# Optimization experiments

Measured on AMD Instinct MI355X. Metric: run time of the kernel, lower is better.

## Reference

```python
import jax, jax.numpy as jnp
import numpy as np

B, N, C, D = 16, 1024, 768, 384

def setup_inputs() -> dict:
    key = jax.random.key(0)
    ks = jax.random.split(key, 12)
    s_in = 1.0 / np.sqrt(C)
    s_d = 1.0 / np.sqrt(D)
    return {
        "x": jax.random.normal(ks[0], (B, N, C), dtype=jnp.float32),
        "adj": jax.random.uniform(ks[1], (B, N, N), dtype=jnp.float32),
        "W_theta": jax.random.uniform(ks[2], (C, D), minval=-s_in, maxval=s_in),
        "b_theta": jax.random.uniform(ks[3], (D,), minval=-s_in, maxval=s_in),
        "W_phi": jax.random.uniform(ks[4], (C, D), minval=-s_in, maxval=s_in),
        "b_phi": jax.random.uniform(ks[5], (D,), minval=-s_in, maxval=s_in),
        "W_g": jax.random.uniform(ks[6], (C, D), minval=-s_in, maxval=s_in),
        "b_g": jax.random.uniform(ks[7], (D,), minval=-s_in, maxval=s_in),
        "W_out": jax.random.uniform(ks[8], (D, C), minval=-s_d, maxval=s_d),
        "b_out": jax.random.uniform(ks[9], (C,), minval=-s_d, maxval=s_d),
    }

def reference(x, adj, W_theta, b_theta, W_phi, b_phi, W_g, b_g, W_out, b_out):
    # projections: [B,N,C] @ [C,D] -> [B,N,D]
    theta = x @ W_theta + b_theta
    phi = x @ W_phi + b_phi
    g = x @ W_g + b_g
    # unscaled attention scores with multiplicative adjacency mask
    attn = jnp.einsum('bnd,bmd->bnm', theta, phi) * adj  # [B,N,N]
    attn = jax.nn.softmax(attn, axis=-1)  # dropout is identity in eval mode
    out = jnp.einsum('bnm,bmd->bnd', attn, g)  # [B,N,D]
    out = out @ W_out + b_out  # [B,N,C]
    return out + x
```

## Files before the change

kernel.cpp:

```cpp
#include <hip/hip_runtime.h>
#include <hip/hip_bf16.h>

typedef __hip_bfloat16 bf16;
typedef short bf16x8 __attribute__((ext_vector_type(8)));
typedef float f32x4 __attribute__((ext_vector_type(4)));

constexpr int Bb = 16, Nn = 1024, Cc = 768, Dd = 384;

static __device__ __forceinline__ f32x4 mfma16(bf16x8 a, bf16x8 b, f32x4 c) {
    return __builtin_amdgcn_mfma_f32_16x16x32_bf16(a, b, c, 0, 0, 0);
}
static __device__ __forceinline__ short f2b(float v) {
    __hip_bfloat16 h = __float2bfloat16(v);
    return *reinterpret_cast<short*>(&h);
}
static __device__ __forceinline__ float b2f(bf16 x) { return __bfloat162float(x); }
static __device__ __forceinline__ float ldf(const float* p) { return *p; }
static __device__ __forceinline__ float ldf(const bf16* p) { return __bfloat162float(*p); }

__global__ __launch_bounds__(256) void transpose_cast(
    const float* __restrict__ in, bf16* __restrict__ out, int K, int N)
{
    __shared__ float t[32][33];
    const int n0 = blockIdx.x * 32, k0 = blockIdx.y * 32;
    const int tx = threadIdx.x & 31, ty = threadIdx.x >> 5;
#pragma unroll
    for (int i = 0; i < 4; i++)
        t[ty + i * 8][tx] = in[(size_t)(k0 + ty + i * 8) * N + n0 + tx];
    __syncthreads();
#pragma unroll
    for (int i = 0; i < 4; i++)
        out[(size_t)(n0 + ty + i * 8) * K + k0 + tx] = __float2bfloat16(t[tx][ty + i * 8]);
}

template <typename TA, int EPI>
__global__ __launch_bounds__(256) void gemm_mfma(
    const TA* __restrict__ A, const bf16* __restrict__ BT,
    const float* __restrict__ bias, const float* __restrict__ resid,
    void* __restrict__ outp, int K, int Nout)
{
    __shared__ short As[128 * 40];
    __shared__ short Bs[128 * 40];
    const int tid = threadIdx.x;
    const int lane = tid & 63, w = tid >> 6;
    const int quad = lane >> 4, c = lane & 15;
    const int row0 = blockIdx.x * 128, col0 = blockIdx.y * 128;
    const int wm = (w & 1) * 64, wn = (w >> 1) * 64;

    const f32x4 fz = {0.f, 0.f, 0.f, 0.f};
    f32x4 acc[4][4];
#pragma unroll
    for (int i = 0; i < 4; i++)
#pragma unroll
        for (int j = 0; j < 4; j++) acc[i][j] = fz;

    for (int k0 = 0; k0 < K; k0 += 32) {
        __syncthreads();
        if (sizeof(TA) == 4) {
            const float* Af = (const float*)A;
#pragma unroll
            for (int u = 0; u < 4; u++) {
                const int id = u * 256 + tid;
                const int r = id >> 3, c4 = (id & 7) * 4;
                const float4 v = *reinterpret_cast<const float4*>(Af + (size_t)(row0 + r) * K + k0 + c4);
                uint2 p;
                p.x = ((unsigned)(unsigned short)f2b(v.y) << 16) | (unsigned short)(unsigned)f2b(v.x);
                p.y = ((unsigned)(unsigned short)f2b(v.w) << 16) | (unsigned short)(unsigned)f2b(v.z);
                *reinterpret_cast<uint2*>(&As[r * 40 + c4]) = p;
            }
        } else {
            const bf16* Ab = (const bf16*)A;
#pragma unroll
            for (int u = 0; u < 2; u++) {
                const int id = u * 256 + tid;
                const int r = id >> 2, c8 = (id & 3) * 8;
                const uint4 v = *reinterpret_cast<const uint4*>(Ab + (size_t)(row0 + r) * K + k0 + c8);
                *reinterpret_cast<uint4*>(&As[r * 40 + c8]) = v;
            }
        }
#pragma unroll
        for (int u = 0; u < 2; u++) {
            const int id = u * 256 + tid;
            const int r = id >> 2, c8 = (id & 3) * 8;
            const uint4 v = *reinterpret_cast<const uint4*>(BT + (size_t)(col0 + r) * K + k0 + c8);
            *reinterpret_cast<uint4*>(&Bs[r * 40 + c8]) = v;
        }
        __syncthreads();

        bf16x8 af[4], bfr[4];
#pragma unroll
        for (int i = 0; i < 4; i++)
            af[i] = *reinterpret_cast<const bf16x8*>(&As[(wm + i * 16 + c) * 40 + quad * 8]);
#pragma unroll
        for (int j = 0; j < 4; j++)
            bfr[j] = *reinterpret_cast<const bf16x8*>(&Bs[(wn + j * 16 + c) * 40 + quad * 8]);
#pragma unroll
        for (int i = 0; i < 4; i++)
#pragma unroll
            for (int j = 0; j < 4; j++)
                acc[i][j] = mfma16(af[i], bfr[j], acc[i][j]);
    }

#pragma unroll
    for (int i = 0; i < 4; i++) {
        const int rowb = row0 + wm + i * 16 + quad * 4;
#pragma unroll
        for (int j = 0; j < 4; j++) {
            const int col = col0 + wn + j * 16 + c;
            const float bcol = bias[col];
#pragma unroll
            for (int r = 0; r < 4; r++) {
                float v = acc[i][j][r] + bcol;
                const int rr = rowb + r;
                if (EPI == 0) {
                    ((bf16*)outp)[(size_t)rr * Nout + col] = __float2bfloat16(v);
                } else if (EPI == 1) {
                    const int bb = rr >> 10, m = rr & 1023;
                    ((bf16*)outp)[((size_t)(bb * Nout + col)) * 1024 + m] = __float2bfloat16(v);
                } else {
                    v += resid[(size_t)rr * Nout + col];
                    ((float*)outp)[(size_t)rr * Nout + col] = v;
                }
            }
        }
    }
}

__global__ __launch_bounds__(256) void flash_attn(
    const bf16* __restrict__ theta, const bf16* __restrict__ phi,
    const bf16* __restrict__ gT, const float* __restrict__ adj,
    bf16* __restrict__ O)
{
    __shared__ short phs[32 * 392];
    __shared__ short gts[384 * 40];
    __shared__ short pls[4][16 * 40];

    const int tid = threadIdx.x;
    const int lane = tid & 63, w = tid >> 6;
    const int quad = lane >> 4, c = lane & 15;
    const int qb = blockIdx.x, b = blockIdx.y;

    const size_t thbase = ((size_t)b * Nn + qb * 64 + w * 16 + c) * Dd;
    bf16x8 ath[12];
#pragma unroll
    for (int dq = 0; dq < 12; dq++)
        ath[dq] = *reinterpret_cast<const bf16x8*>(theta + thbase + dq * 32 + quad * 8);

    const f32x4 fz = {0.f, 0.f, 0.f, 0.f};
    f32x4 o[24];
#pragma unroll
    for (int t = 0; t < 24; t++) o[t] = fz;
    float mrow[4], lrow[4];
#pragma unroll
    for (int r = 0; r < 4; r++) { mrow[r] = -INFINITY; lrow[r] = 0.f; }

    for (int n0 = 0; n0 < Nn; n0 += 32) {
        __syncthreads();
        {
            const bf16* src = phi + ((size_t)b * Nn + n0) * Dd;
#pragma unroll
            for (int u = 0; u < 6; u++) {
                const int id = u * 256 + tid;
                const int r = id / 48, cc = (id % 48) * 8;
                const uint4 v = *reinterpret_cast<const uint4*>(src + (size_t)r * Dd + cc);
                *reinterpret_cast<uint4*>(&phs[r * 392 + cc]) = v;
            }
        }
        {
            const bf16* src = gT + ((size_t)b * Dd) * Nn + n0;
#pragma unroll
            for (int u = 0; u < 6; u++) {
                const int id = u * 256 + tid;
                const int r = id >> 2, cc = (id & 3) * 8;
                const uint4 v = *reinterpret_cast<const uint4*>(src + (size_t)r * Nn + cc);
                *reinterpret_cast<uint4*>(&gts[r * 40 + cc]) = v;
            }
        }
        __syncthreads();

        f32x4 s0 = fz, s1 = fz;
#pragma unroll
        for (int dq = 0; dq < 12; dq++) {
            const bf16x8 b0 = *reinterpret_cast<const bf16x8*>(&phs[c * 392 + dq * 32 + quad * 8]);
            const bf16x8 b1 = *reinterpret_cast<const bf16x8*>(&phs[(16 + c) * 392 + dq * 32 + quad * 8]);
            s0 = mfma16(ath[dq], b0, s0);
            s1 = mfma16(ath[dq], b1, s1);
        }

        const float* arow = adj + ((size_t)b * Nn + qb * 64 + w * 16 + quad * 4) * Nn + n0;
        float p0[4], p1[4], alpha[4];
#pragma unroll
        for (int r = 0; r < 4; r++) {
            const float v0 = s0[r] * arow[(size_t)r * Nn + c];
            const float v1 = s1[r] * arow[(size_t)r * Nn + 16 + c];
            float t = fmaxf(v0, v1);
#pragma unroll
            for (int msk = 1; msk < 16; msk <<= 1) t = fmaxf(t, __shfl_xor(t, msk));
            const float mn = fmaxf(mrow[r], t);
            alpha[r] = __expf(mrow[r] - mn);
            mrow[r] = mn;
            p0[r] = __expf(v0 - mn);
            p1[r] = __expf(v1 - mn);
            float u = p0[r] + p1[r];
#pragma unroll
            for (int msk = 1; msk < 16; msk <<= 1) u += __shfl_xor(u, msk);
            lrow[r] = lrow[r] * alpha[r] + u;
        }
#pragma unroll
        for (int t = 0; t < 24; t++)
#pragma unroll
            for (int r = 0; r < 4; r++) o[t][r] *= alpha[r];

        short* pl = (short*)pls[w];
#pragma unroll
        for (int r = 0; r < 4; r++) {
            pl[(quad * 4 + r) * 40 + c] = f2b(p0[r]);
            pl[(quad * 4 + r) * 40 + 16 + c] = f2b(p1[r]);
        }
        __syncthreads();
        const bf16x8 ap = *reinterpret_cast<const bf16x8*>(&pl[c * 40 + quad * 8]);
#pragma unroll
        for (int dn = 0; dn < 24; dn++) {
            const bf16x8 bg = *reinterpret_cast<const bf16x8*>(&gts[(dn * 16 + c) * 40 + quad * 8]);
            o[dn] = mfma16(ap, bg, o[dn]);
        }
    }

    float inv[4];
#pragma unroll
    for (int r = 0; r < 4; r++) inv[r] = 1.0f / lrow[r];
    bf16* orow = O + ((size_t)b * Nn + qb * 64 + w * 16 + quad * 4) * Dd;
#pragma unroll
    for (int dn = 0; dn < 24; dn++)
#pragma unroll
        for (int r = 0; r < 4; r++)
            orow[(size_t)r * Dd + dn * 16 + c] = __float2bfloat16(o[dn][r] * inv[r]);
}

__global__ __launch_bounds__(256) void proj_gemm(
    const float* __restrict__ A, const float* __restrict__ W,
    const float* __restrict__ bias, bf16* __restrict__ out,
    int M, int K, int Nd)
{
    __shared__ float Asm[16][65];
    __shared__ float Bsm[16][65];
    const int tid = threadIdx.x;
    const int tx = tid & 15, ty = tid >> 4;
    const int row0 = blockIdx.x * 64, col0 = blockIdx.y * 64;
    float acc[4][4] = {};
    for (int k0 = 0; k0 < K; k0 += 16) {
        {
            const int m = tid >> 2, kq = (tid & 3) * 4;
            const float* p = A + (size_t)(row0 + m) * K + k0 + kq;
#pragma unroll
            for (int j = 0; j < 4; j++) Asm[kq + j][m] = p[j];
        }
        {
            const int k = tid >> 4, n4 = (tid & 15) * 4;
            const float* p = W + (size_t)(k0 + k) * Nd + col0 + n4;
#pragma unroll
            for (int j = 0; j < 4; j++) Bsm[k][n4 + j] = p[j];
        }
        __syncthreads();
#pragma unroll
        for (int k = 0; k < 16; k++) {
            float a[4], bv[4];
#pragma unroll
            for (int j = 0; j < 4; j++) a[j] = Asm[k][ty * 4 + j];
#pragma unroll
            for (int j = 0; j < 4; j++) bv[j] = Bsm[k][tx * 4 + j];
#pragma unroll
            for (int i = 0; i < 4; i++)
#pragma unroll
                for (int j = 0; j < 4; j++) acc[i][j] += a[i] * bv[j];
        }
        __syncthreads();
    }
#pragma unroll
    for (int i = 0; i < 4; i++) {
        const int row = row0 + ty * 4 + i;
#pragma unroll
        for (int j = 0; j < 4; j++) {
            const int col = col0 + tx * 4 + j;
            out[(size_t)row * Nd + col] = __float2bfloat16(acc[i][j] + bias[col]);
        }
    }
}

__global__ __launch_bounds__(256) void fused_attn(
    const float* __restrict__ x, const float* __restrict__ adj,
    const float* __restrict__ W_theta, const float* __restrict__ b_theta,
    const bf16* __restrict__ phi, const bf16* __restrict__ g,
    const float* __restrict__ W_out, const float* __restrict__ b_out,
    float* __restrict__ out)
{
    __shared__ float xs[Cc];
    __shared__ float th[Dd];
    __shared__ float s[Nn];
    __shared__ float Os[Dd];
    __shared__ float red[256];
    const int tid = threadIdx.x;
    const int n = blockIdx.x, b = blockIdx.y;
    const int lane = tid & 63, wave = tid >> 6;
    const size_t row = (size_t)b * Nn + n;
    const size_t baseD = (size_t)b * Nn * Dd;
    for (int c = tid; c < Cc; c += 256) xs[c] = x[row * Cc + c];
    __syncthreads();
    for (int d = tid; d < Dd; d += 256) {
        float acc = b_theta[d];
#pragma unroll 8
        for (int c = 0; c < Cc; c++) acc += xs[c] * W_theta[(size_t)c * Dd + d];
        th[d] = acc;
    }
    __syncthreads();
    for (int m = wave; m < Nn; m += 4) {
        const bf16* prow = phi + baseD + (size_t)m * Dd;
        float partial = 0.f;
#pragma unroll
        for (int j = 0; j < 6; j++) {
            const int d = lane + 64 * j;
            partial += th[d] * b2f(prow[d]);
        }
#pragma unroll
        for (int off = 32; off > 0; off >>= 1) partial += __shfl_down(partial, off);
        if (lane == 0)
            s[m] = partial * adj[(size_t)b * Nn * Nn + (size_t)n * Nn + m];
    }
    __syncthreads();
    float mx = -1e30f;
    for (int i = tid; i < Nn; i += 256) mx = fmaxf(mx, s[i]);
    red[tid] = mx; __syncthreads();
    for (int st = 128; st > 0; st >>= 1) {
        if (tid < st) red[tid] = fmaxf(red[tid], red[tid + st]);
        __syncthreads();
    }
    mx = red[0]; __syncthreads();
    float lsum = 0.f;
    for (int i = tid; i < Nn; i += 256) {
        const float e = __expf(s[i] - mx);
        s[i] = e;
        lsum += e;
    }
    red[tid] = lsum; __syncthreads();
    for (int st = 128; st > 0; st >>= 1) {
        if (tid < st) red[tid] += red[tid + st];
        __syncthreads();
    }
    const float inv = 1.0f / red[0];
    __syncthreads();
    for (int d = tid; d < Dd; d += 256) {
        float acc = 0.f;
#pragma unroll 8
        for (int m = 0; m < Nn; m++) acc += s[m] * b2f(g[baseD + (size_t)m * Dd + d]);
        Os[d] = acc * inv;
    }
    __syncthreads();
    for (int c = tid; c < Cc; c += 256) {
        float acc = b_out[c] + xs[c];
#pragma unroll 8
        for (int d = 0; d < Dd; d++) acc += Os[d] * W_out[(size_t)d * Cc + c];
        out[row * Cc + c] = acc;
    }
}

extern "C" void kernel_launch(void* const* d_in, const int* in_sizes, int n_in,
                              void* d_out, int out_size, void* d_ws, size_t ws_size,
                              hipStream_t stream)
{
    const float* x       = (const float*)d_in[0];
    const float* adj     = (const float*)d_in[1];
    const float* W_theta = (const float*)d_in[2];
    const float* b_theta = (const float*)d_in[3];
    const float* W_phi   = (const float*)d_in[4];
    const float* b_phi   = (const float*)d_in[5];
    const float* W_g     = (const float*)d_in[6];
    const float* b_g     = (const float*)d_in[7];
    const float* W_out   = (const float*)d_in[8];
    const float* b_out   = (const float*)d_in[9];
    float* out = (float*)d_out;

    const int M = Bb * Nn;
    const size_t SZ = (size_t)Bb * Nn * Dd;
    const size_t WSZ = (size_t)Cc * Dd;
    const size_t NEED = (4 * WSZ + 4 * SZ) * sizeof(bf16);

    dim3 blk(256);

    if (ws_size >= NEED) {
        bf16* WtT   = (bf16*)d_ws;
        bf16* WpT   = WtT + WSZ;
        bf16* WgT   = WpT + WSZ;
        bf16* WoT   = WgT + WSZ;
        bf16* theta = WoT + WSZ;
        bf16* phi   = theta + SZ;
        bf16* gT    = phi + SZ;
        bf16* O     = gT + SZ;

        transpose_cast<<<dim3(Dd / 32, Cc / 32), blk, 0, stream>>>(W_theta, WtT, Cc, Dd);
        transpose_cast<<<dim3(Dd / 32, Cc / 32), blk, 0, stream>>>(W_phi,   WpT, Cc, Dd);
        transpose_cast<<<dim3(Dd / 32, Cc / 32), blk, 0, stream>>>(W_g,     WgT, Cc, Dd);
        transpose_cast<<<dim3(Cc / 32, Dd / 32), blk, 0, stream>>>(W_out,   WoT, Dd, Cc);

        dim3 gp(M / 128, Dd / 128);
        gemm_mfma<float, 0><<<gp, blk, 0, stream>>>(x, WtT, b_theta, nullptr, theta, Cc, Dd);
        gemm_mfma<float, 0><<<gp, blk, 0, stream>>>(x, WpT, b_phi,   nullptr, phi,   Cc, Dd);
        gemm_mfma<float, 1><<<gp, blk, 0, stream>>>(x, WgT, b_g,     nullptr, gT,    Cc, Dd);

        flash_attn<<<dim3(Nn / 64, Bb), blk, 0, stream>>>(theta, phi, gT, adj, O);

        dim3 go(M / 128, Cc / 128);
        gemm_mfma<bf16, 2><<<go, blk, 0, stream>>>(O, WoT, b_out, x, out, Dd, Cc);
    } else {
        bf16* phi = (bf16*)d_ws;
        bf16* g   = phi + SZ;
        dim3 gproj(M / 64, Dd / 64);
        proj_gemm<<<gproj, blk, 0, stream>>>(x, W_phi, b_phi, phi, M, Cc, Dd);
        proj_gemm<<<gproj, blk, 0, stream>>>(x, W_g, b_g, g, M, Cc, Dd);
        fused_attn<<<dim3(Nn, Bb), blk, 0, stream>>>(
            x, adj, W_theta, b_theta, phi, g, W_out, b_out, out);
    }
}
```

Before: 375.7 us.

## Fuse QKV projections into one GEMM and double-buffer attention tile loads

Casts x to bf16 once and runs a single GEMM against the contiguous transposed weights (N=1152), with a new epilogue that scatters results into theta, phi and transposed g. This replaces three separate projection launches that each re-read fp32 x. The flash attention kernel now double-buffers the phi and gT tiles in LDS and prefetches the next tile and the adj values into registers, which removes one barrier per iteration. In exchange it uses more LDS and registers (launch_bounds 256,1) and needs extra workspace for the bf16 copy of x.

```diff
diff --git a/kernel.cpp b/kernel.cpp
--- a/kernel.cpp
+++ b/kernel.cpp
@@ -14,9 +14,34 @@
     __hip_bfloat16 h = __float2bfloat16(v);
     return *reinterpret_cast<short*>(&h);
 }
+static __device__ __forceinline__ unsigned pack2(float lo, float hi) {
+    return ((unsigned)(unsigned short)f2b(hi) << 16) | (unsigned short)(unsigned)f2b(lo);
+}
 static __device__ __forceinline__ float b2f(bf16 x) { return __bfloat162float(x); }
-static __device__ __forceinline__ float ldf(const float* p) { return *p; }
-static __device__ __forceinline__ float ldf(const bf16* p) { return __bfloat162float(*p); }
+
+__global__ __launch_bounds__(256) void cast_bf16(
+    const float* __restrict__ in, uint4* __restrict__ out)
+{
+    const size_t i = (size_t)blockIdx.x * 256 + threadIdx.x;
+    const float4 a = reinterpret_cast<const float4*>(in)[i * 2];
+    const float4 b = reinterpret_cast<const float4*>(in)[i * 2 + 1];
+    uint4 v;
+    v.x = pack2(a.x, a.y);
+    v.y = pack2(a.z, a.w);
+    v.z = pack2(b.x, b.y);
+    v.w = pack2(b.z, b.w);
+    out[i] = v;
+}
+
+__global__ __launch_bounds__(256) void pack_bias(
+    const float* __restrict__ bt, const float* __restrict__ bp,
+    const float* __restrict__ bg, float* __restrict__ out)
+{
+    const int i = blockIdx.x * 256 + threadIdx.x;
+    if (i < 384) out[i] = bt[i];
+    else if (i < 768) out[i] = bp[i - 384];
+    else if (i < 1152) out[i] = bg[i - 768];
+}
 
 __global__ __launch_bounds__(256) void transpose_cast(
     const float* __restrict__ in, bf16* __restrict__ out, int K, int N)
@@ -64,8 +89,8 @@
                 const int r = id >> 3, c4 = (id & 7) * 4;
                 const float4 v = *reinterpret_cast<const float4*>(Af + (size_t)(row0 + r) * K + k0 + c4);
                 uint2 p;
-                p.x = ((unsigned)(unsigned short)f2b(v.y) << 16) | (unsigned short)(unsigned)f2b(v.x);
-                p.y = ((unsigned)(unsigned short)f2b(v.w) << 16) | (unsigned short)(unsigned)f2b(v.z);
+                p.x = pack2(v.x, v.y);
+                p.y = pack2(v.z, v.w);
                 *reinterpret_cast<uint2*>(&As[r * 40 + c4]) = p;
             }
         } else {
@@ -101,6 +126,7 @@
                 acc[i][j] = mfma16(af[i], bfr[j], acc[i][j]);
     }
 
+    const size_t SZc = (size_t)Bb * Nn * Dd;
 #pragma unroll
     for (int i = 0; i < 4; i++) {
         const int rowb = row0 + wm + i * 16 + quad * 4;
@@ -117,22 +143,32 @@
                 } else if (EPI == 1) {
                     const int bb = rr >> 10, m = rr & 1023;
                     ((bf16*)outp)[((size_t)(bb * Nout + col)) * 1024 + m] = __float2bfloat16(v);
-                } else {
+                } else if (EPI == 2) {
                     v += resid[(size_t)rr * Nout + col];
                     ((float*)outp)[(size_t)rr * Nout + col] = v;
+                } else {
+                    const int seg = col / 384;
+                    const int cl = col - seg * 384;
+                    bf16* base = (bf16*)outp;
+                    if (seg < 2) {
+                        base[(size_t)seg * SZc + (size_t)rr * Dd + cl] = __float2bfloat16(v);
+                    } else {
+                        const int bb = rr >> 10, m = rr & 1023;
+                        base[2 * SZc + ((size_t)(bb * Dd + cl)) * 1024 + m] = __float2bfloat16(v);
+                    }
                 }
             }
         }
     }
 }
 
-__global__ __launch_bounds__(256) void flash_attn(
+__global__ __launch_bounds__(256, 1) void flash_attn(
     const bf16* __restrict__ theta, const bf16* __restrict__ phi,
     const bf16* __restrict__ gT, const float* __restrict__ adj,
     bf16* __restrict__ O)
 {
-    __shared__ short phs[32 * 392];
-    __shared__ short gts[384 * 40];
+    __shared__ short phs[2][32 * 392];
+    __shared__ short gts[2][384 * 40];
     __shared__ short pls[4][16 * 40];
 
     const int tid = threadIdx.x;
@@ -146,6 +182,33 @@
     for (int dq = 0; dq < 12; dq++)
         ath[dq] = *reinterpret_cast<const bf16x8*>(theta + thbase + dq * 32 + quad * 8);
 
+    const bf16* phibase = phi + (size_t)b * Nn * Dd;
+    const bf16* gtb = gT + (size_t)b * Dd * Nn;
+    const float* arow = adj + ((size_t)b * Nn + qb * 64 + w * 16 + quad * 4) * Nn;
+
+    uint4 vph[6], vgt[6];
+    float av0[4], av1[4];
+
+    auto prefetch = [&](int n0) {
+#pragma unroll
+        for (int u = 0; u < 6; u++) {
+            const int id = u * 256 + tid;
+            vph[u] = *reinterpret_cast<const uint4*>(
+                phibase + (size_t)(n0 + id / 48) * Dd + (id % 48) * 8);
+        }
+#pragma unroll
+        for (int u = 0; u < 6; u++) {
+            const int id = u * 256 + tid;
+            vgt[u] = *reinterpret_cast<const uint4*>(
+                gtb + (size_t)(id >> 2) * Nn + n0 + (id & 3) * 8);
+        }
+#pragma unroll
+        for (int r = 0; r < 4; r++) {
+            av0[r] = arow[(size_t)r * Nn + n0 + c];
+            av1[r] = arow[(size_t)r * Nn + n0 + 16 + c];
+        }
+    };
+
     const f32x4 fz = {0.f, 0.f, 0.f, 0.f};
     f32x4 o[24];
 #pragma unroll
@@ -154,45 +217,45 @@
 #pragma unroll
     for (int r = 0; r < 4; r++) { mrow[r] = -INFINITY; lrow[r] = 0.f; }
 
-    for (int n0 = 0; n0 < Nn; n0 += 32) {
-        __syncthreads();
-        {
-            const bf16* src = phi + ((size_t)b * Nn + n0) * Dd;
-#pragma unroll
-            for (int u = 0; u < 6; u++) {
-                const int id = u * 256 + tid;
-                const int r = id / 48, cc = (id % 48) * 8;
-                const uint4 v = *reinterpret_cast<const uint4*>(src + (size_t)r * Dd + cc);
-                *reinterpret_cast<uint4*>(&phs[r * 392 + cc]) = v;
-            }
-        }
-        {
-            const bf16* src = gT + ((size_t)b * Dd) * Nn + n0;
-#pragma unroll
-            for (int u = 0; u < 6; u++) {
-                const int id = u * 256 + tid;
-                const int r = id >> 2, cc = (id & 3) * 8;
-                const uint4 v = *reinterpret_cast<const uint4*>(src + (size_t)r * Nn + cc);
-                *reinterpret_cast<uint4*>(&gts[r * 40 + cc]) = v;
-            }
-        }
+    prefetch(0);
+
+    for (int it = 0; it < 32; ++it) {
+        const int n0 = it * 32;
+        short* ph = (short*)phs[it & 1];
+        short* gt = (short*)gts[it & 1];
+
+#pragma unroll
+        for (int u = 0; u < 6; u++) {
+            const int id = u * 256 + tid;
+            *reinterpret_cast<uint4*>(&ph[(id / 48) * 392 + (id % 48) * 8]) = vph[u];
+        }
+#pragma unroll
+        for (int u = 0; u < 6; u++) {
+            const int id = u * 256 + tid;
+            *reinterpret_cast<uint4*>(&gt[(id >> 2) * 40 + (id & 3) * 8]) = vgt[u];
+        }
+        float a0[4], a1[4];
+#pragma unroll
+        for (int r = 0; r < 4; r++) { a0[r] = av0[r]; a1[r] = av1[r]; }
+
+        if (it < 31) prefetch(n0 + 32);
+
         __syncthreads();
 
         f32x4 s0 = fz, s1 = fz;
 #pragma unroll
         for (int dq = 0; dq < 12; dq++) {
-            const bf16x8 b0 = *reinterpret_cast<const bf16x8*>(&phs[c * 392 + dq * 32 + quad * 8]);
-            const bf16x8 b1 = *reinterpret_cast<const bf16x8*>(&phs[(16 + c) * 392 + dq * 32 + quad * 8]);
+            const bf16x8 b0 = *reinterpret_cast<const bf16x8*>(&ph[c * 392 + dq * 32 + quad * 8]);
+            const bf16x8 b1 = *reinterpret_cast<const bf16x8*>(&ph[(16 + c) * 392 + dq * 32 + quad * 8]);
             s0 = mfma16(ath[dq], b0, s0);
             s1 = mfma16(ath[dq], b1, s1);
         }
 
-        const float* arow = adj + ((size_t)b * Nn + qb * 64 + w * 16 + quad * 4) * Nn + n0;
         float p0[4], p1[4], alpha[4];
 #pragma unroll
         for (int r = 0; r < 4; r++) {
-            const float v0 = s0[r] * arow[(size_t)r * Nn + c];
-            const float v1 = s1[r] * arow[(size_t)r * Nn + 16 + c];
+            const float v0 = s0[r] * a0[r];
+            const float v1 = s1[r] * a1[r];
             float t = fmaxf(v0, v1);
 #pragma unroll
             for (int msk = 1; msk < 16; msk <<= 1) t = fmaxf(t, __shfl_xor(t, msk));
@@ -217,11 +280,10 @@
             pl[(quad * 4 + r) * 40 + c] = f2b(p0[r]);
             pl[(quad * 4 + r) * 40 + 16 + c] = f2b(p1[r]);
         }
-        __syncthreads();
         const bf16x8 ap = *reinterpret_cast<const bf16x8*>(&pl[c * 40 + quad * 8]);
 #pragma unroll
         for (int dn = 0; dn < 24; dn++) {
-            const bf16x8 bg = *reinterpret_cast<const bf16x8*>(&gts[(dn * 16 + c) * 40 + quad * 8]);
+            const bf16x8 bg = *reinterpret_cast<const bf16x8*>(&gt[(dn * 16 + c) * 40 + quad * 8]);
             o[dn] = mfma16(ap, bg, o[dn]);
         }
     }
@@ -380,13 +442,42 @@
     float* out = (float*)d_out;
 
     const int M = Bb * Nn;
-    const size_t SZ = (size_t)Bb * Nn * Dd;
+    const size_t SZ  = (size_t)Bb * Nn * Dd;
+    const size_t SZX = (size_t)M * Cc;
     const size_t WSZ = (size_t)Cc * Dd;
-    const size_t NEED = (4 * WSZ + 4 * SZ) * sizeof(bf16);
+    const size_t NEED_OLD = (4 * WSZ + 4 * SZ) * sizeof(bf16);
+    const size_t NEED_NEW = (4 * WSZ + 4 * SZ + SZX) * sizeof(bf16)
+                          + 1152 * sizeof(float);
 
     dim3 blk(256);
 
-    if (ws_size >= NEED) {
+    if (ws_size >= NEED_NEW) {
+        bf16* WtT   = (bf16*)d_ws;
+        bf16* WpT   = WtT + WSZ;
+        bf16* WgT   = WpT + WSZ;
+        bf16* WoT   = WgT + WSZ;
+        bf16* theta = WoT + WSZ;
+        bf16* phi   = theta + SZ;
+        bf16* gT    = phi + SZ;
+        bf16* O     = gT + SZ;
+        bf16* xb    = O + SZ;
+        float* biasP = (float*)(xb + SZX);
+
+        cast_bf16<<<dim3((unsigned)(SZX / 2048)), blk, 0, stream>>>(x, (uint4*)xb);
+        transpose_cast<<<dim3(Dd / 32, Cc / 32), blk, 0, stream>>>(W_theta, WtT, Cc, Dd);
+        transpose_cast<<<dim3(Dd / 32, Cc / 32), blk, 0, stream>>>(W_phi,   WpT, Cc, Dd);
+        transpose_cast<<<dim3(Dd / 32, Cc / 32), blk, 0, stream>>>(W_g,     WgT, Cc, Dd);
+        transpose_cast<<<dim3(Cc / 32, Dd / 32), blk, 0, stream>>>(W_out,   WoT, Dd, Cc);
+        pack_bias<<<dim3(5), blk, 0, stream>>>(b_theta, b_phi, b_g, biasP);
+
+        gemm_mfma<bf16, 3><<<dim3(M / 128, 1152 / 128), blk, 0, stream>>>(
+            xb, WtT, biasP, nullptr, theta, Cc, 1152);
+
+        flash_attn<<<dim3(Nn / 64, Bb), blk, 0, stream>>>(theta, phi, gT, adj, O);
+
+        gemm_mfma<bf16, 2><<<dim3(M / 128, Cc / 128), blk, 0, stream>>>(
+            O, WoT, b_out, x, out, Dd, Cc);
+    } else if (ws_size >= NEED_OLD) {
         bf16* WtT   = (bf16*)d_ws;
         bf16* WpT   = WtT + WSZ;
         bf16* WgT   = WpT + WSZ;
```

Result: slower. 391.7 us (+4.3%).
